# Performance work log

Measured on AMD Instinct MI355X. Metric: run time of the kernel, lower is better.

The kernel has to match this reference:

```python
import jax, jax.numpy as jnp
import numpy as np

N = 100000
E = 1600000
F_FEAT, F_COND, F_HID, F_LAT = 128, 32, 128, 64


def setup_inputs() -> dict:
    key = jax.random.key(0)
    ks = jax.random.split(key, 16)
    feature = jax.random.normal(ks[0], (N, F_FEAT), dtype=jnp.float32)
    condition = jax.random.normal(ks[1], (N, F_COND), dtype=jnp.float32)
    edge_index = jax.random.randint(ks[2], (2, E), 0, N, dtype=jnp.int64)

    def glorot(k, fan_in, fan_out):
        s = jnp.sqrt(6.0 / (fan_in + fan_out)).astype(jnp.float32)
        return jax.random.uniform(k, (fan_in, fan_out), jnp.float32, -s, s)

    enc_in = F_FEAT + F_COND   # 160
    dec_in = F_LAT + F_COND    # 96
    return {
        "feature": feature,
        "condition": condition,
        "edge_index": edge_index,
        "W_e1": glorot(ks[3], enc_in, F_HID), "b_e1": jnp.zeros((F_HID,), jnp.float32),
        "W_e2": glorot(ks[4], F_HID, F_HID), "b_e2": jnp.zeros((F_HID,), jnp.float32),
        "W_e3": glorot(ks[5], F_HID, F_LAT), "b_e3": jnp.zeros((F_LAT,), jnp.float32),
        "W_d1": glorot(ks[6], dec_in, F_HID), "b_d1": jnp.zeros((F_HID,), jnp.float32),
        "W_d2": glorot(ks[7], F_HID, F_HID), "b_d2": jnp.zeros((F_HID,), jnp.float32),
        "W_d3": glorot(ks[8], F_HID, F_FEAT), "b_d3": jnp.zeros((F_FEAT,), jnp.float32),
    }


def _gcn_conv(x, W, b, src, dst, dinv):
    # GCNConv with add_self_loops=True, symmetric normalization:
    # out = D^{-1/2} (A + I) D^{-1/2} X W + b
    h = x @ W                                        # [N, out]
    coef = (dinv[src] * dinv[dst])[:, None]          # [E, 1]
    msg = h[src] * coef                              # [E, out]
    agg = jax.ops.segment_sum(msg, dst, num_segments=x.shape[0])
    agg = agg + h * (dinv * dinv)[:, None]           # self-loop term
    return agg + b


def reference(feature, condition, edge_index,
              W_e1, b_e1, W_e2, b_e2, W_e3, b_e3,
              W_d1, b_d1, W_d2, b_d2, W_d3, b_d3):
    src, dst = edge_index[0], edge_index[1]
    n = feature.shape[0]
    # degree with self loops (edge weights = 1)
    deg = jax.ops.segment_sum(jnp.ones((src.shape[0],), jnp.float32), dst,
                              num_segments=n) + 1.0
    dinv = jax.lax.rsqrt(deg)

    # encoder
    x = jnp.concatenate([feature, condition], axis=1)
    h = jnp.tanh(_gcn_conv(x, W_e1, b_e1, src, dst, dinv))
    h = jnp.tanh(_gcn_conv(h, W_e2, b_e2, src, dst, dinv))
    z = _gcn_conv(h, W_e3, b_e3, src, dst, dinv)

    # decoder
    x = jnp.concatenate([z, condition], axis=1)
    h = jnp.tanh(_gcn_conv(x, W_d1, b_d1, src, dst, dinv))
    h = jnp.tanh(_gcn_conv(h, W_d2, b_d2, src, dst, dinv))
    out = _gcn_conv(h, W_d3, b_d3, src, dst, dinv)
    return out
```

## Files before the change

### kernel.cpp

```cpp
#include <hip/hip_runtime.h>
#include <hip/hip_fp16.h>
#include <math.h>

#define NN 100000
#define NE 1600000
#define NB ((NN + 255) >> 8)
#define CHUNK 8192
#define CAP 8192

typedef __attribute__((ext_vector_type(4))) float floatx4;
typedef __attribute__((ext_vector_type(8))) short shortx8;


__global__ __launch_bounds__(256)
void coarse_hist(const int* __restrict__ ei, int* __restrict__ bucket_cnt, int E) {
    __shared__ int h[512];
    int t = threadIdx.x;
    for (int i = t; i < 512; i += 256) h[i] = 0;
    __syncthreads();
    int base = blockIdx.x * CHUNK;
    int lim = min(base + CHUNK, E);
    for (int e = base + t; e < lim; e += 256) {
        int d = ei[E + e];
        atomicAdd(&h[d >> 8], 1);
    }
    __syncthreads();
    for (int i = t; i < 512; i += 256)
        if (h[i]) atomicAdd(&bucket_cnt[i], h[i]);
}

__global__ void scan_buckets(const int* __restrict__ bucket_cnt,
                             int* __restrict__ bucket_base,
                             int* __restrict__ bucket_fill) {
    __shared__ int sh[512];
    int t = threadIdx.x;
    int v = (t < NB) ? bucket_cnt[t] : 0;
    sh[t] = v;
    __syncthreads();
    for (int off = 1; off < 512; off <<= 1) {
        int u = (t >= off) ? sh[t - off] : 0;
        __syncthreads();
        sh[t] += u;
        __syncthreads();
    }
    int ex = (t == 0) ? 0 : sh[t - 1];
    if (t <= NB) bucket_base[t] = ex;
    if (t < NB) bucket_fill[t] = ex;
}

__global__ __launch_bounds__(256)
void coarse_scatter(const int* __restrict__ ei, int* __restrict__ bucket_fill,
                    unsigned long long* __restrict__ pairs, int E) {
    __shared__ int h[512];
    __shared__ int base[512];
    int t = threadIdx.x;
    for (int i = t; i < 512; i += 256) h[i] = 0;
    __syncthreads();
    int cbase = blockIdx.x * CHUNK;
    int lim = min(cbase + CHUNK, E);
    for (int e = cbase + t; e < lim; e += 256) {
        int d = ei[E + e];
        atomicAdd(&h[d >> 8], 1);
    }
    __syncthreads();
    for (int i = t; i < 512; i += 256)
        base[i] = h[i] ? atomicAdd(&bucket_fill[i], h[i]) : 0;
    __syncthreads();
    for (int i = t; i < 512; i += 256) h[i] = 0;
    __syncthreads();
    for (int e = cbase + t; e < lim; e += 256) {
        int s = ei[e];
        int d = ei[E + e];
        int b = d >> 8;
        int r = atomicAdd(&h[b], 1);
        pairs[base[b] + r] =
            ((unsigned long long)(unsigned)d << 32) | (unsigned)s;
    }
}

__global__ __launch_bounds__(256)
void fine_csr(const unsigned long long* __restrict__ pairs,
              const int* __restrict__ bucket_base,
              int* __restrict__ rowptr, int* __restrict__ colid,
              float* __restrict__ dinv, int n) {
    __shared__ int hist[256];
    __shared__ int offs[256];
    __shared__ int rank[256];
    __shared__ int lbuf[CAP];
    int b = blockIdx.x, t = threadIdx.x;
    int beg = bucket_base[b], end = bucket_base[b + 1];
    int cnt = end - beg;
    hist[t] = 0; rank[t] = 0;
    __syncthreads();
    for (int i = t; i < cnt; i += 256) {
        int d = (int)(pairs[beg + i] >> 32);
        atomicAdd(&hist[d & 255], 1);
    }
    __syncthreads();
    int v = hist[t];
    offs[t] = v;
    __syncthreads();
    for (int off = 1; off < 256; off <<= 1) {
        int u = (t >= off) ? offs[t - off] : 0;
        __syncthreads();
        offs[t] += u;
        __syncthreads();
    }
    int ex = (t == 0) ? 0 : offs[t - 1];
    int node = (b << 8) + t;
    if (node < n) {
        rowptr[node] = beg + ex;
        dinv[node] = rsqrtf((float)v + 1.0f);
    } else if (node == n) {
        rowptr[n] = beg + ex;
    }
    __syncthreads();
    offs[t] = ex;
    __syncthreads();
    for (int i = t; i < cnt; i += 256) {
        unsigned long long p = pairs[beg + i];
        int d = (int)(p >> 32) & 255;
        int s = (int)(p & 0xffffffffu);
        int r = atomicAdd(&rank[d], 1);
        lbuf[offs[d] + r] = s;
    }
    __syncthreads();
    for (int i = t; i < cnt; i += 256) colid[beg + i] = lbuf[i];
}


__global__ void concat_kernel(const float4* __restrict__ f, const float4* __restrict__ c,
                              float4* __restrict__ A, int n) {
    int i = blockIdx.x * 256 + threadIdx.x;
    int total = n * 40;
    if (i < total) {
        int row = i / 40, j = i % 40;
        A[i] = (j < 32) ? f[row * 32 + j] : c[row * 8 + (j - 32)];
    }
}

__global__ void condcopy_kernel(const float4* __restrict__ c, float4* __restrict__ A, int n) {
    int i = blockIdx.x * 256 + threadIdx.x;
    if (i < n * 8) {
        int row = i / 8, j = i % 8;
        A[row * 24 + 16 + j] = c[row * 8 + j];
    }
}


__global__ void wsplit_kernel(const float* __restrict__ W,
                              unsigned short* __restrict__ Wsw,
                              int K, int OUT) {
    int i = blockIdx.x * 256 + threadIdx.x;
    if (i < K * OUT) {
        int k = i / OUT, o = i % OUT;
        float w = W[i];
        unsigned u = __float_as_uint(w);
        float r = w - __uint_as_float(u & 0xFFFF0000u);
        int NT = OUT >> 4;
        int ktc = k >> 5, q = (k >> 3) & 3, j = k & 7;
        int nt = o >> 4, m = o & 15;
        int lane = (q << 4) | m;
        size_t base = ((((size_t)(ktc * NT + nt) * 2) * 64 + lane) << 3) + j;
        Wsw[base] = (unsigned short)(u >> 16);
        Wsw[base + 512] = (unsigned short)(__float_as_uint(r) >> 16);
    }
}


__device__ __forceinline__ void split8(const float* v, shortx8& hi, shortx8& lo) {
#pragma unroll
    for (int i = 0; i < 8; i++) {
        unsigned u = __float_as_uint(v[i]);
        float r = v[i] - __uint_as_float(u & 0xFFFF0000u);
        hi[i] = (short)(u >> 16);
        lo[i] = (short)(__float_as_uint(r) >> 16);
    }
}

template <int OUT, int K>
__global__ __launch_bounds__(512)
void gemm_mfma(const float* __restrict__ X,
               const unsigned short* __restrict__ Wsw,
               const float* __restrict__ dinv,
               __half* __restrict__ Y, int ntiles) {
    constexpr int NT = OUT / 16;
    constexpr int NKTC = K / 32;
    constexpr int PERC = OUT * 128;
    constexpr int CSZ = (65536 / PERC < NKTC) ? (65536 / PERC) : NKTC;
    __shared__ __align__(16) unsigned short lds[CSZ * PERC / 2];

    const int t = threadIdx.x;
    const int wave = t >> 6, lane = t & 63;
    const int m = lane & 15, q = lane >> 4;
    const int tile = blockIdx.x * 8 + wave;
    const bool act = tile < ntiles;
    const int row = act ? tile * 16 + m : 0;
    const float* ap = X + (size_t)row * K + q * 8;

    floatx4 acc[NT];
#pragma unroll
    for (int nt = 0; nt < NT; nt++) acc[nt] = (floatx4){0.f, 0.f, 0.f, 0.f};

#pragma unroll
    for (int c0 = 0; c0 < NKTC; c0 += CSZ) {
        const int cl = (NKTC - c0 < CSZ) ? (NKTC - c0) : CSZ;
        if (c0 != 0) __syncthreads();
        {
            const float4* gs = (const float4*)Wsw + (size_t)c0 * (PERC / 16);
            float4* ld = (float4*)lds;
            int tot = cl * (PERC / 16);
            for (int i = t; i < tot; i += 512) ld[i] = gs[i];
        }
        __syncthreads();
        if (act) {
#pragma unroll
            for (int ktc = 0; ktc < cl; ktc++) {
                int kg = (c0 + ktc) * 32;
                float av[8];
                *(float4*)&av[0] = *(const float4*)(ap + kg);
                *(float4*)&av[4] = *(const float4*)(ap + kg + 4);
                shortx8 ahi, alo;
                split8(av, ahi, alo);
#pragma unroll
                for (int nt = 0; nt < NT; nt++) {
                    const unsigned short* fb =
                        lds + ((((ktc * NT + nt) * 2) * 64 + lane) << 3);
                    shortx8 bhi = *(const shortx8*)fb;
                    shortx8 blo = *(const shortx8*)(fb + 512);
                    acc[nt] = __builtin_amdgcn_mfma_f32_16x16x32_bf16(ahi, bhi, acc[nt], 0, 0, 0);
                    acc[nt] = __builtin_amdgcn_mfma_f32_16x16x32_bf16(ahi, blo, acc[nt], 0, 0, 0);
                    acc[nt] = __builtin_amdgcn_mfma_f32_16x16x32_bf16(alo, bhi, acc[nt], 0, 0, 0);
                }
            }
        }
    }

    if (act) {
        float di[4];
#pragma unroll
        for (int r = 0; r < 4; r++) di[r] = dinv[tile * 16 + q * 4 + r];
#pragma unroll
        for (int nt = 0; nt < NT; nt++) {
#pragma unroll
            for (int r = 0; r < 4; r++) {
                int orow = tile * 16 + q * 4 + r;
                Y[(size_t)orow * OUT + nt * 16 + m] = __float2half_rn(acc[nt][r] * di[r]);
            }
        }
    }
}


template <int OUT, bool TANH>
__global__ __launch_bounds__(256)
void prop_kernel(const __half* __restrict__ hs, const float* __restrict__ dinv,
                 const int* __restrict__ rowptr, const int* __restrict__ colid,
                 const float* __restrict__ bias,
                 float* __restrict__ out, int ldo, int n) {
    int wave = threadIdx.x >> 6;
    int lane = threadIdx.x & 63;
    int node = blockIdx.x * 4 + wave;
    if (node >= n) return;
    int beg = rowptr[node], end = rowptr[node + 1];

    if constexpr (OUT == 128) {
        const __half2* base = (const __half2*)hs;
        float2 self = __half22float2(base[(size_t)node * 64 + lane]);
        float accx = self.x, accy = self.y;
        float accx2 = 0.f, accy2 = 0.f;
        int e = beg;
        for (; e + 8 <= end; e += 8) {
            int s[8];
#pragma unroll
            for (int j = 0; j < 8; j++) s[j] = colid[e + j];
            __half2 v[8];
#pragma unroll
            for (int j = 0; j < 8; j++) v[j] = base[(size_t)s[j] * 64 + lane];
#pragma unroll
            for (int j = 0; j < 8; j += 2) {
                float2 f0 = __half22float2(v[j]);
                float2 f1 = __half22float2(v[j + 1]);
                accx += f0.x; accy += f0.y;
                accx2 += f1.x; accy2 += f1.y;
            }
        }
        if (e + 4 <= end) {
            int s[4];
#pragma unroll
            for (int j = 0; j < 4; j++) s[j] = colid[e + j];
            __half2 v[4];
#pragma unroll
            for (int j = 0; j < 4; j++) v[j] = base[(size_t)s[j] * 64 + lane];
            float2 f0 = __half22float2(v[0]), f1 = __half22float2(v[1]);
            float2 f2 = __half22float2(v[2]), f3 = __half22float2(v[3]);
            accx += f0.x + f2.x; accy += f0.y + f2.y;
            accx2 += f1.x + f3.x; accy2 += f1.y + f3.y;
            e += 4;
        }
        for (; e < end; e++) {
            float2 f = __half22float2(base[(size_t)colid[e] * 64 + lane]);
            accx += f.x; accy += f.y;
        }
        accx += accx2; accy += accy2;
        float di = dinv[node];
        float ox = di * accx + bias[2 * lane];
        float oy = di * accy + bias[2 * lane + 1];
        if (TANH) { ox = tanhf(ox); oy = tanhf(oy); }
        *(float2*)(out + (size_t)node * ldo + 2 * lane) = make_float2(ox, oy);
    } else {
        float acc = __half2float(hs[(size_t)node * 64 + lane]);
        float acc2 = 0.f;
        int e = beg;
        for (; e + 8 <= end; e += 8) {
            int s[8];
#pragma unroll
            for (int j = 0; j < 8; j++) s[j] = colid[e + j];
            __half v[8];
#pragma unroll
            for (int j = 0; j < 8; j++) v[j] = hs[(size_t)s[j] * 64 + lane];
#pragma unroll
            for (int j = 0; j < 8; j += 2) {
                acc += __half2float(v[j]);
                acc2 += __half2float(v[j + 1]);
            }
        }
        if (e + 4 <= end) {
            int s[4];
#pragma unroll
            for (int j = 0; j < 4; j++) s[j] = colid[e + j];
            __half v[4];
#pragma unroll
            for (int j = 0; j < 4; j++) v[j] = hs[(size_t)s[j] * 64 + lane];
            acc += __half2float(v[0]) + __half2float(v[2]);
            acc2 += __half2float(v[1]) + __half2float(v[3]);
            e += 4;
        }
        for (; e < end; e++) acc += __half2float(hs[(size_t)colid[e] * 64 + lane]);
        acc += acc2;
        float v = dinv[node] * acc + bias[lane];
        if (TANH) v = tanhf(v);
        out[(size_t)node * ldo + lane] = v;
    }
}


extern "C" void kernel_launch(void* const* d_in, const int* in_sizes, int n_in,
                              void* d_out, int out_size, void* d_ws, size_t ws_size,
                              hipStream_t stream) {
    const int n = NN, E = NE;
    const float* feature   = (const float*)d_in[0];
    const float* condition = (const float*)d_in[1];
    const int*   ei        = (const int*)d_in[2];
    const float* W_e1 = (const float*)d_in[3];  const float* b_e1 = (const float*)d_in[4];
    const float* W_e2 = (const float*)d_in[5];  const float* b_e2 = (const float*)d_in[6];
    const float* W_e3 = (const float*)d_in[7];  const float* b_e3 = (const float*)d_in[8];
    const float* W_d1 = (const float*)d_in[9];  const float* b_d1 = (const float*)d_in[10];
    const float* W_d2 = (const float*)d_in[11]; const float* b_d2 = (const float*)d_in[12];
    const float* W_d3 = (const float*)d_in[13]; const float* b_d3 = (const float*)d_in[14];
    float* out = (float*)d_out;

    float*  A    = (float*)d_ws;
    __half* H16  = (__half*)(A + (size_t)n * 160);
    float*  dinv = (float*)(H16 + (size_t)n * 128);
    int* rowptr  = (int*)(dinv + n);
    int* colid   = rowptr + n + 1;
    uintptr_t pp = (uintptr_t)(colid + E);
    pp = (pp + 15) & ~(uintptr_t)15;
    unsigned long long* pairs = (unsigned long long*)pp;
    int* bucket_cnt  = (int*)(pairs + E);
    int* bucket_base = bucket_cnt + 512;
    int* bucket_fill = bucket_base + 512;
    uintptr_t wp = (uintptr_t)(bucket_fill + 512);
    wp = (wp + 15) & ~(uintptr_t)15;
    unsigned short* wt = (unsigned short*)wp;
    unsigned short* e1w = wt;             unsigned short* e2w = e1w + 160 * 128 * 2;
    unsigned short* e3w = e2w + 128*128*2; unsigned short* d1w = e3w + 128 * 64 * 2;
    unsigned short* d2w = d1w + 96*128*2;  unsigned short* d3w = d2w + 128 * 128 * 2;

    hipMemsetAsync(bucket_cnt, 0, 512 * sizeof(int), stream);

    int nbc = (E + CHUNK - 1) / CHUNK;
    coarse_hist<<<nbc, 256, 0, stream>>>(ei, bucket_cnt, E);
    scan_buckets<<<1, 512, 0, stream>>>(bucket_cnt, bucket_base, bucket_fill);
    coarse_scatter<<<nbc, 256, 0, stream>>>(ei, bucket_fill, pairs, E);
    fine_csr<<<NB, 256, 0, stream>>>(pairs, bucket_base, rowptr, colid, dinv, n);

    wsplit_kernel<<<(160*128 + 255)/256, 256, 0, stream>>>(W_e1, e1w, 160, 128);
    wsplit_kernel<<<(128*128 + 255)/256, 256, 0, stream>>>(W_e2, e2w, 128, 128);
    wsplit_kernel<<<(128*64  + 255)/256, 256, 0, stream>>>(W_e3, e3w, 128, 64);
    wsplit_kernel<<<(96*128  + 255)/256, 256, 0, stream>>>(W_d1, d1w, 96, 128);
    wsplit_kernel<<<(128*128 + 255)/256, 256, 0, stream>>>(W_d2, d2w, 128, 128);
    wsplit_kernel<<<(128*128 + 255)/256, 256, 0, stream>>>(W_d3, d3w, 128, 128);

    concat_kernel<<<(n * 40 + 255) / 256, 256, 0, stream>>>(
        (const float4*)feature, (const float4*)condition, (float4*)A, n);

    const int ntiles = n / 16;
    const int gb = (ntiles + 7) / 8;
    int pb = (n + 3) / 4;

    gemm_mfma<128, 160><<<gb, 512, 0, stream>>>(A, e1w, dinv, H16, ntiles);
    prop_kernel<128, true><<<pb, 256, 0, stream>>>(H16, dinv, rowptr, colid, b_e1, A, 128, n);
    gemm_mfma<128, 128><<<gb, 512, 0, stream>>>(A, e2w, dinv, H16, ntiles);
    prop_kernel<128, true><<<pb, 256, 0, stream>>>(H16, dinv, rowptr, colid, b_e2, A, 128, n);
    gemm_mfma<64, 128><<<gb, 512, 0, stream>>>(A, e3w, dinv, H16, ntiles);
    prop_kernel<64, false><<<pb, 256, 0, stream>>>(H16, dinv, rowptr, colid, b_e3, A, 96, n);
    condcopy_kernel<<<(n * 8 + 255) / 256, 256, 0, stream>>>(
        (const float4*)condition, (float4*)A, n);

    gemm_mfma<128, 96><<<gb, 512, 0, stream>>>(A, d1w, dinv, H16, ntiles);
    prop_kernel<128, true><<<pb, 256, 0, stream>>>(H16, dinv, rowptr, colid, b_d1, A, 128, n);
    gemm_mfma<128, 128><<<gb, 512, 0, stream>>>(A, d2w, dinv, H16, ntiles);
    prop_kernel<128, true><<<pb, 256, 0, stream>>>(H16, dinv, rowptr, colid, b_d2, A, 128, n);
    gemm_mfma<128, 128><<<gb, 512, 0, stream>>>(A, d3w, dinv, H16, ntiles);
    prop_kernel<128, false><<<pb, 256, 0, stream>>>(H16, dinv, rowptr, colid, b_d3, out, 128, n);
}
```

Before: 730.8 us.

## Store GEMM output in 16-column chunks and gather per chunk in propagation

The GEMM now writes its fp16 output in a column-chunked layout, [chunk][node][16]. Propagation launches one block per chunk per group of nodes, so each gather touches a smaller working set that is more likely to stay in cache. Inside a wave, eight edge slots are handled in parallel and combined with cross-lane shuffles. The concat and condition-copy kernels are removed: the GEMM reads its two inputs directly from separate pointers. The cost is more blocks and repeated reads of rowptr and colid for every chunk.

```diff
diff --git a/kernel.cpp b/kernel.cpp
--- a/kernel.cpp
+++ b/kernel.cpp
@@ -129,25 +129,6 @@
 }
 
 
-__global__ void concat_kernel(const float4* __restrict__ f, const float4* __restrict__ c,
-                              float4* __restrict__ A, int n) {
-    int i = blockIdx.x * 256 + threadIdx.x;
-    int total = n * 40;
-    if (i < total) {
-        int row = i / 40, j = i % 40;
-        A[i] = (j < 32) ? f[row * 32 + j] : c[row * 8 + (j - 32)];
-    }
-}
-
-__global__ void condcopy_kernel(const float4* __restrict__ c, float4* __restrict__ A, int n) {
-    int i = blockIdx.x * 256 + threadIdx.x;
-    if (i < n * 8) {
-        int row = i / 8, j = i % 8;
-        A[row * 24 + 16 + j] = c[row * 8 + j];
-    }
-}
-
-
 __global__ void wsplit_kernel(const float* __restrict__ W,
                               unsigned short* __restrict__ Wsw,
                               int K, int OUT) {
@@ -159,8 +140,8 @@
         float r = w - __uint_as_float(u & 0xFFFF0000u);
         int NT = OUT >> 4;
         int ktc = k >> 5, q = (k >> 3) & 3, j = k & 7;
-        int nt = o >> 4, m = o & 15;
-        int lane = (q << 4) | m;
+        int nt = o >> 4, mm = o & 15;
+        int lane = (q << 4) | mm;
         size_t base = ((((size_t)(ktc * NT + nt) * 2) * 64 + lane) << 3) + j;
         Wsw[base] = (unsigned short)(u >> 16);
         Wsw[base + 512] = (unsigned short)(__float_as_uint(r) >> 16);
@@ -178,14 +159,15 @@
     }
 }
 
-template <int OUT, int K>
+template <int OUT, int K, int K1>
 __global__ __launch_bounds__(512)
-void gemm_mfma(const float* __restrict__ X,
+void gemm_mfma(const float* __restrict__ X1, const float* __restrict__ X2,
                const unsigned short* __restrict__ Wsw,
                const float* __restrict__ dinv,
                __half* __restrict__ Y, int ntiles) {
     constexpr int NT = OUT / 16;
     constexpr int NKTC = K / 32;
+    constexpr int K2 = K - K1;
     constexpr int PERC = OUT * 128;
     constexpr int CSZ = (65536 / PERC < NKTC) ? (65536 / PERC) : NKTC;
     __shared__ __align__(16) unsigned short lds[CSZ * PERC / 2];
@@ -196,7 +178,9 @@
     const int tile = blockIdx.x * 8 + wave;
     const bool act = tile < ntiles;
     const int row = act ? tile * 16 + m : 0;
-    const float* ap = X + (size_t)row * K + q * 8;
+    const int nfull = ntiles * 16;
+    const float* ap1 = X1 + (size_t)row * K1 + q * 8;
+    const float* ap2 = (K2 > 0) ? (X2 + (size_t)row * K2 + q * 8) : X1;
 
     floatx4 acc[NT];
 #pragma unroll
@@ -216,10 +200,11 @@
         if (act) {
 #pragma unroll
             for (int ktc = 0; ktc < cl; ktc++) {
-                int kg = (c0 + ktc) * 32;
+                const int kg = (c0 + ktc) * 32;
+                const float* p = (kg < K1) ? (ap1 + kg) : (ap2 + (kg - K1));
                 float av[8];
-                *(float4*)&av[0] = *(const float4*)(ap + kg);
-                *(float4*)&av[4] = *(const float4*)(ap + kg + 4);
+                *(float4*)&av[0] = *(const float4*)(p);
+                *(float4*)&av[4] = *(const float4*)(p + 4);
                 shortx8 ahi, alo;
                 split8(av, ahi, alo);
 #pragma unroll
@@ -245,102 +230,60 @@
 #pragma unroll
             for (int r = 0; r < 4; r++) {
                 int orow = tile * 16 + q * 4 + r;
-                Y[(size_t)orow * OUT + nt * 16 + m] = __float2half_rn(acc[nt][r] * di[r]);
+                Y[((size_t)nt * nfull + orow) * 16 + m] =
+                    __float2half_rn(acc[nt][r] * di[r]);
             }
         }
     }
 }
 
 
-template <int OUT, bool TANH>
-__global__ __launch_bounds__(256)
-void prop_kernel(const __half* __restrict__ hs, const float* __restrict__ dinv,
-                 const int* __restrict__ rowptr, const int* __restrict__ colid,
-                 const float* __restrict__ bias,
-                 float* __restrict__ out, int ldo, int n) {
-    int wave = threadIdx.x >> 6;
-    int lane = threadIdx.x & 63;
-    int node = blockIdx.x * 4 + wave;
+template <int NCH, bool TANH>
+__global__ __launch_bounds__(512)
+void prop_chunk(const __half2* __restrict__ hs, const float* __restrict__ dinv,
+                const int* __restrict__ rowptr, const int* __restrict__ colid,
+                const float* __restrict__ bias, float* __restrict__ out,
+                int ldo, int n) {
+    int bid = blockIdx.x;
+    int c = bid & (NCH - 1);
+    int nb = bid / NCH;
+    int wave = threadIdx.x >> 6, lane = threadIdx.x & 63;
+    int node = nb * 8 + wave;
     if (node >= n) return;
+    int slot = lane >> 3, f = lane & 7;
     int beg = rowptr[node], end = rowptr[node + 1];
-
-    if constexpr (OUT == 128) {
-        const __half2* base = (const __half2*)hs;
-        float2 self = __half22float2(base[(size_t)node * 64 + lane]);
-        float accx = self.x, accy = self.y;
-        float accx2 = 0.f, accy2 = 0.f;
-        int e = beg;
-        for (; e + 8 <= end; e += 8) {
-            int s[8];
-#pragma unroll
-            for (int j = 0; j < 8; j++) s[j] = colid[e + j];
-            __half2 v[8];
-#pragma unroll
-            for (int j = 0; j < 8; j++) v[j] = base[(size_t)s[j] * 64 + lane];
-#pragma unroll
-            for (int j = 0; j < 8; j += 2) {
-                float2 f0 = __half22float2(v[j]);
-                float2 f1 = __half22float2(v[j + 1]);
-                accx += f0.x; accy += f0.y;
-                accx2 += f1.x; accy2 += f1.y;
-            }
-        }
-        if (e + 4 <= end) {
-            int s[4];
-#pragma unroll
-            for (int j = 0; j < 4; j++) s[j] = colid[e + j];
-            __half2 v[4];
-#pragma unroll
-            for (int j = 0; j < 4; j++) v[j] = base[(size_t)s[j] * 64 + lane];
-            float2 f0 = __half22float2(v[0]), f1 = __half22float2(v[1]);
-            float2 f2 = __half22float2(v[2]), f3 = __half22float2(v[3]);
-            accx += f0.x + f2.x; accy += f0.y + f2.y;
-            accx2 += f1.x + f3.x; accy2 += f1.y + f3.y;
-            e += 4;
-        }
-        for (; e < end; e++) {
-            float2 f = __half22float2(base[(size_t)colid[e] * 64 + lane]);
-            accx += f.x; accy += f.y;
-        }
-        accx += accx2; accy += accy2;
-        float di = dinv[node];
-        float ox = di * accx + bias[2 * lane];
-        float oy = di * accy + bias[2 * lane + 1];
-        if (TANH) { ox = tanhf(ox); oy = tanhf(oy); }
-        *(float2*)(out + (size_t)node * ldo + 2 * lane) = make_float2(ox, oy);
-    } else {
-        float acc = __half2float(hs[(size_t)node * 64 + lane]);
-        float acc2 = 0.f;
-        int e = beg;
-        for (; e + 8 <= end; e += 8) {
-            int s[8];
-#pragma unroll
-            for (int j = 0; j < 8; j++) s[j] = colid[e + j];
-            __half v[8];
-#pragma unroll
-            for (int j = 0; j < 8; j++) v[j] = hs[(size_t)s[j] * 64 + lane];
-#pragma unroll
-            for (int j = 0; j < 8; j += 2) {
-                acc += __half2float(v[j]);
-                acc2 += __half2float(v[j + 1]);
-            }
-        }
-        if (e + 4 <= end) {
-            int s[4];
-#pragma unroll
-            for (int j = 0; j < 4; j++) s[j] = colid[e + j];
-            __half v[4];
-#pragma unroll
-            for (int j = 0; j < 4; j++) v[j] = hs[(size_t)s[j] * 64 + lane];
-            acc += __half2float(v[0]) + __half2float(v[2]);
-            acc2 += __half2float(v[1]) + __half2float(v[3]);
-            e += 4;
-        }
-        for (; e < end; e++) acc += __half2float(hs[(size_t)colid[e] * 64 + lane]);
-        acc += acc2;
-        float v = dinv[node] * acc + bias[lane];
-        if (TANH) v = tanhf(v);
-        out[(size_t)node * ldo + lane] = v;
+    const __half2* __restrict__ base = hs + (size_t)c * n * 8;
+
+    float ax = 0.f, ay = 0.f, bx = 0.f, by = 0.f;
+    int e = beg + slot;
+    for (; e + 8 < end; e += 16) {
+        int s0 = __builtin_nontemporal_load(colid + e);
+        int s1 = __builtin_nontemporal_load(colid + e + 8);
+        float2 v0 = __half22float2(base[(unsigned)(s0 * 8 + f)]);
+        float2 v1 = __half22float2(base[(unsigned)(s1 * 8 + f)]);
+        ax += v0.x; ay += v0.y; bx += v1.x; by += v1.y;
+    }
+    if (e < end) {
+        int s = __builtin_nontemporal_load(colid + e);
+        float2 v = __half22float2(base[(unsigned)(s * 8 + f)]);
+        ax += v.x; ay += v.y;
+    }
+    ax += bx; ay += by;
+    ax += __shfl_xor(ax, 8);  ay += __shfl_xor(ay, 8);
+    ax += __shfl_xor(ax, 16); ay += __shfl_xor(ay, 16);
+    ax += __shfl_xor(ax, 32); ay += __shfl_xor(ay, 32);
+
+    float2 sf = __half22float2(base[(unsigned)(node * 8 + f)]);
+    float di = dinv[node];
+    float2 bb = *(const float2*)(bias + c * 16 + 2 * f);
+    float ox = di * (ax + sf.x) + bb.x;
+    float oy = di * (ay + sf.y) + bb.y;
+    if (TANH) { ox = tanhf(ox); oy = tanhf(oy); }
+    if (slot == 0) {
+        union { float2 f2; unsigned long long u; } cv;
+        cv.f2 = make_float2(ox, oy);
+        __builtin_nontemporal_store(
+            cv.u, (unsigned long long*)(out + (size_t)node * ldo + c * 16 + 2 * f));
     }
 }
 
@@ -374,7 +317,7 @@
     uintptr_t wp = (uintptr_t)(bucket_fill + 512);
     wp = (wp + 15) & ~(uintptr_t)15;
     unsigned short* wt = (unsigned short*)wp;
-    unsigned short* e1w = wt;             unsigned short* e2w = e1w + 160 * 128 * 2;
+    unsigned short* e1w = wt;              unsigned short* e2w = e1w + 160 * 128 * 2;
     unsigned short* e3w = e2w + 128*128*2; unsigned short* d1w = e3w + 128 * 64 * 2;
     unsigned short* d2w = d1w + 96*128*2;  unsigned short* d3w = d2w + 128 * 128 * 2;
 
@@ -393,26 +336,21 @@
     wsplit_kernel<<<(128*128 + 255)/256, 256, 0, stream>>>(W_d2, d2w, 128, 128);
     wsplit_kernel<<<(128*128 + 255)/256, 256, 0, stream>>>(W_d3, d3w, 128, 128);
 
-    concat_kernel<<<(n * 40 + 255) / 256, 256, 0, stream>>>(
-        (const float4*)feature, (const float4*)condition, (float4*)A, n);
-
     const int ntiles = n / 16;
     const int gb = (ntiles + 7) / 8;
-    int pb = (n + 3) / 4;
-
-    gemm_mfma<128, 160><<<gb, 512, 0, stream>>>(A, e1w, dinv, H16, ntiles);
-    prop_kernel<128, true><<<pb, 256, 0, stream>>>(H16, dinv, rowptr, colid, b_e1, A, 128, n);
-    gemm_mfma<128, 128><<<gb, 512, 0, stream>>>(A, e2w, dinv, H16, ntiles);
-    prop_kernel<128, true><<<pb, 256, 0, stream>>>(H16, dinv, rowptr, colid, b_e2, A, 128, n);
-    gemm_mfma<64, 128><<<gb, 512, 0, stream>>>(A, e3w, dinv, H16, ntiles);
-    prop_kernel<64, false><<<pb, 256, 0, stream>>>(H16, dinv, rowptr, colid, b_e3, A, 96, n);
-    condcopy_kernel<<<(n * 8 + 255) / 256, 256, 0, stream>>>(
-        (const float4*)condition, (float4*)A, n);
-
-    gemm_mfma<128, 96><<<gb, 512, 0, stream>>>(A, d1w, dinv, H16, ntiles);
-    prop_kernel<128, true><<<pb, 256, 0, stream>>>(H16, dinv, rowptr, colid, b_d1, A, 128, n);
-    gemm_mfma<128, 128><<<gb, 512, 0, stream>>>(A, d2w, dinv, H16, ntiles);
-    prop_kernel<128, true><<<pb, 256, 0, stream>>>(H16, dinv, rowptr, colid, b_d2, A, 128, n);
-    gemm_mfma<128, 128><<<gb, 512, 0, stream>>>(A, d3w, dinv, H16, ntiles);
-    prop_kernel<128, false><<<pb, 256, 0, stream>>>(H16, dinv, rowptr, colid, b_d3, out, 128, n);
-}
+    const int pnb = (n + 7) / 8;
+
+    gemm_mfma<128, 160, 128><<<gb, 512, 0, stream>>>(feature, condition, e1w, dinv, H16, ntiles);
+    prop_chunk<8, true><<<8 * pnb, 512, 0, stream>>>((const __half2*)H16, dinv, rowptr, colid, b_e1, A, 128, n);
+    gemm_mfma<128, 128, 128><<<gb, 512, 0, stream>>>(A, nullptr, e2w, dinv, H16, ntiles);
+    prop_chunk<8, true><<<8 * pnb, 512, 0, stream>>>((const __half2*)H16, dinv, rowptr, colid, b_e2, A, 128, n);
+    gemm_mfma<64, 128, 128><<<gb, 512, 0, stream>>>(A, nullptr, e3w, dinv, H16, ntiles);
+    prop_chunk<4, false><<<4 * pnb, 512, 0, stream>>>((const __half2*)H16, dinv, rowptr, colid, b_e3, A, 64, n);
+
+    gemm_mfma<128, 96, 64><<<gb, 512, 0, stream>>>(A, condition, d1w, dinv, H16, ntiles);
+    prop_chunk<8, true><<<8 * pnb, 512, 0, stream>>>((const __half2*)H16, dinv, rowptr, colid, b_d1, A, 128, n);
+    gemm_mfma<128, 128, 128><<<gb, 512, 0, stream>>>(A, nullptr, d2w, dinv, H16, ntiles);
+    prop_chunk<8, true><<<8 * pnb, 512, 0, stream>>>((const __half2*)H16, dinv, rowptr, colid, b_d2, A, 128, n);
+    gemm_mfma<128, 128, 128><<<gb, 512, 0, stream>>>(A, nullptr, d3w, dinv, H16, ntiles);
+    prop_chunk<8, false><<<8 * pnb, 512, 0, stream>>>((const __half2*)H16, dinv, rowptr, colid, b_d3, out, 128, n);
+}
```

Result: slower. 1.783 ms (+143.9%).
